# Kernel optimization log

Measured on AMD Instinct MI355X. Metric: run time of the kernel, lower is better.

The kernel has to match this reference:

```python
import jax, jax.numpy as jnp
import numpy as np

WS = 7          # window size
DISP = 3        # WS // 2 cyclic shift displacement
HEADS = 3
HD = 32         # head dim
DIM = 96        # hidden dim (= HEADS*HD)
DS = 4          # patch-merging downscale factor
NWH = 16        # windows per spatial dim after merging (112/7)
SCALE = HD ** -0.5


def _rel_indices(ws):
    idx = np.array([[x, y] for x in range(ws) for y in range(ws)])
    return idx[None, :, :] - idx[:, None, :] + ws - 1  # (ws^2, ws^2, 2)


def _shift_mask(ws, disp, nwh, nww):
    n = ws * ws
    ul = np.zeros((n, n), np.float32)
    ul[-disp * ws:, :-disp * ws] = -np.inf
    ul[:-disp * ws, -disp * ws:] = -np.inf
    lr = np.zeros((ws, ws, ws, ws), np.float32)
    lr[:, -disp:, :, :-disp] = -np.inf
    lr[:, :-disp, :, -disp:] = -np.inf
    lr = lr.reshape(n, n)
    m = np.zeros((nwh * nww, n, n), np.float32)
    m[-nww:] += ul            # last row of windows: upper/lower mask
    m[nww - 1::nww] += lr     # last column of windows: left/right mask
    return m

REL = jnp.asarray(_rel_indices(WS))                       # (49,49,2) int
SHIFT_MASK = jnp.asarray(_shift_mask(WS, DISP, NWH, NWH))  # (256,49,49)


def _layernorm(x, g, b):
    mu = jnp.mean(x, axis=-1, keepdims=True)
    var = jnp.var(x, axis=-1, keepdims=True)
    return (x - mu) * jax.lax.rsqrt(var + 1e-5) * g + b


def _window_attention(y, wqkv, pos_tab, wo, bo, shifted):
    # y: (b, nh, nw, DIM)
    if shifted:
        y = jnp.roll(y, (-DISP, -DISP), axis=(1, 2))
    b, nh, nw, _ = y.shape
    nwh, nww = nh // WS, nw // WS
    qkv = y @ wqkv  # (b, nh, nw, 3*DIM); last dim layout [q|k|v]
    qkv = qkv.reshape(b, nwh, WS, nww, WS, 3, HEADS, HD)
    qkv = qkv.transpose(5, 0, 6, 1, 3, 2, 4, 7).reshape(3, b, HEADS, nwh * nww, WS * WS, HD)
    q, k, v = qkv[0], qkv[1], qkv[2]
    dots = jnp.einsum('bhwid,bhwjd->bhwij', q, k) * SCALE  # (b,h,nwin,49,49)
    dots = dots + pos_tab[REL[..., 0], REL[..., 1]]        # relative pos bias
    if shifted:
        dots = dots + SHIFT_MASK[None, None]
    attn = jax.nn.softmax(dots, axis=-1)
    o = jnp.einsum('bhwij,bhwjd->bhwid', attn, v)
    o = o.reshape(b, HEADS, nwh, nww, WS, WS, HD)
    o = o.transpose(0, 2, 4, 3, 5, 1, 6).reshape(b, nh, nw, HEADS * HD)
    o = o @ wo + bo
    if shifted:
        o = jnp.roll(o, (DISP, DISP), axis=(1, 2))
    return o


def setup_inputs() -> dict:
    key = jax.random.key(0)
    ks = jax.random.split(key, 8)
    B, C, H, W = 16, 3, 448, 448
    s = 0.02
    return {
        'x': jax.random.normal(ks[0], (B, C, H, W), jnp.float32),
        'pm_w': jax.random.normal(ks[1], (C * DS * DS, DIM), jnp.float32) * s,
        'pm_b': jnp.zeros((DIM,), jnp.float32),
        'ln1_g': jnp.ones((2, DIM), jnp.float32),
        'ln1_b': jnp.zeros((2, DIM), jnp.float32),
        'qkv_w': jax.random.normal(ks[2], (2, DIM, 3 * HEADS * HD), jnp.float32) * s,
        'pos': jax.random.normal(ks[3], (2, 2 * WS - 1, 2 * WS - 1), jnp.float32),
        'out_w': jax.random.normal(ks[4], (2, HEADS * HD, DIM), jnp.float32) * s,
        'out_b': jnp.zeros((2, DIM), jnp.float32),
        'ln2_g': jnp.ones((2, DIM), jnp.float32),
        'ln2_b': jnp.zeros((2, DIM), jnp.float32),
        'ff1_w': jax.random.normal(ks[5], (2, DIM, 4 * DIM), jnp.float32) * s,
        'ff1_b': jnp.zeros((2, 4 * DIM), jnp.float32),
        'ff2_w': jax.random.normal(ks[6], (2, 4 * DIM, DIM), jnp.float32) * s,
        'ff2_b': jnp.zeros((2, DIM), jnp.float32),
    }


def reference(x, pm_w, pm_b, ln1_g, ln1_b, qkv_w, pos, out_w, out_b,
              ln2_g, ln2_b, ff1_w, ff1_b, ff2_w, ff2_b):
    b, c, h, w = x.shape
    # PatchMerging: Unfold(k=s=DS) orders channels as (c, kh, kw)
    xp = x.reshape(b, c, h // DS, DS, w // DS, DS)
    xp = xp.transpose(0, 2, 4, 1, 3, 5).reshape(b, h // DS, w // DS, c * DS * DS)
    xp = xp @ pm_w + pm_b  # (b, 112, 112, DIM)
    for i, shifted in enumerate((False, True)):
        y = _layernorm(xp, ln1_g[i], ln1_b[i])
        xp = xp + _window_attention(y, qkv_w[i], pos[i], out_w[i], out_b[i], shifted)
        y = _layernorm(xp, ln2_g[i], ln2_b[i])
        y = jax.nn.gelu(y @ ff1_w[i] + ff1_b[i], approximate=False) @ ff2_w[i] + ff2_b[i]
        xp = xp + y
    return xp.transpose(0, 3, 1, 2)  # (b, DIM, 112, 112)
```

## Files before the change

### kernel.cpp

```cpp
#include <hip/hip_runtime.h>
#include <hip/hip_bf16.h>

#define HW 112
#define NPIX (HW*HW)
#define NTOK_TOTAL (16*NPIX)
#define SCALE_ATTN 0.17677669529663689f

typedef short bf16x8 __attribute__((ext_vector_type(8)));
typedef float f32x4 __attribute__((ext_vector_type(4)));

__device__ __forceinline__ short f2bf(float f) {
    __hip_bfloat16 h = __float2bfloat16(f);
    return *reinterpret_cast<short*>(&h);
}

__device__ __forceinline__ float gelu_tanh(float x) {
    float t  = x * x;
    float m1 = fmaf(0.071354816f, t, 1.5957691f);
    float e  = __expf(x * m1);
    float r  = __builtin_amdgcn_rcpf(e + 1.0f);
    return fmaf(-x, r, x);
}

__global__ __launch_bounds__(256) void patch_merge_kernel(
    const float* __restrict__ x, const float* __restrict__ pm_w,
    const float* __restrict__ pm_b, float* __restrict__ xp)
{
    __shared__ float w_lds[48*96];
    __shared__ float in_lds[16*52];
    __shared__ float b_lds[96];
    const int t = threadIdx.x;
    const int jt = blockIdx.x, i = blockIdx.y, b = blockIdx.z;
    const int j0 = jt * 16;

    for (int e = t; e < 48*96; e += 256) w_lds[e] = pm_w[e];
    if (t < 96) b_lds[t] = pm_b[t];
    for (int e = t; e < 768; e += 256) {
        int r = e >> 6, col = e & 63;
        int c = r >> 2, kh = r & 3;
        float v = x[(((size_t)(b*3 + c))*448 + (4*i + kh))*448 + 4*j0 + col];
        in_lds[(col >> 2)*52 + c*16 + kh*4 + (col & 3)] = v;
    }
    __syncthreads();
    for (int e = t; e < 16*96; e += 256) {
        int pos = e / 96, ch = e % 96;
        float acc = b_lds[ch];
        #pragma unroll
        for (int k = 0; k < 48; ++k)
            acc = fmaf(in_lds[pos*52 + k], w_lds[k*96 + ch], acc);
        xp[((size_t)((b*HW + i)*HW) + j0 + pos)*96 + ch] = acc;
    }
}

__global__ __launch_bounds__(256) void prep_weights_kernel(
    const float* __restrict__ ff1, const float* __restrict__ ff2,
    const float* __restrict__ qkv_w, const float* __restrict__ out_w,
    short* __restrict__ w1T, short* __restrict__ w2T,
    short* __restrict__ qkvT, short* __restrict__ outT)
{
    int i = blockIdx.x * 256 + threadIdx.x;
    if (i < 73728) {
        int l = i / 36864, r = i % 36864, n = r / 96, k = r % 96;
        w1T[i] = f2bf(ff1[(size_t)l*36864 + k*384 + n]);
    } else if (i < 147456) {
        int j = i - 73728;
        int l = j / 36864, r = j % 36864, n = r / 384, k = r % 384;
        w2T[j] = f2bf(ff2[(size_t)l*36864 + k*96 + n]);
    } else if (i < 202752) {
        int j = i - 147456;
        int l = j / 27648, r = j % 27648, n = r / 96, k = r % 96;
        qkvT[j] = f2bf(qkv_w[(size_t)l*27648 + k*288 + n]);
    } else if (i < 221184) {
        int j = i - 202752;
        int l = j / 9216, r = j % 9216, n = r / 96, k = r % 96;
        outT[j] = f2bf(out_w[(size_t)l*9216 + k*96 + n]);
    }
}

template<bool SHIFTED>
__global__ __launch_bounds__(192) void attn_mfma_kernel(
    float* __restrict__ xp,
    const float* __restrict__ ln_g, const float* __restrict__ ln_b,
    const short* __restrict__ qkvT,
    const float* __restrict__ pos_tab,
    const short* __restrict__ outT,
    const float* __restrict__ out_b)
{
    __shared__ short bufA[13824];
    __shared__ short qk_s[13824];
    __shared__ short vT_s[6912];
    __shared__ float pos_l[169];
    __shared__ float ob_s[96];
    __shared__ float lng[96], lnb[96];

    const int t = threadIdx.x;
    const int lane = t & 63;
    const int h = t >> 6;
    const int l15 = lane & 15, lhi = lane >> 4;
    const int wh = blockIdx.x >> 4, ww = blockIdx.x & 15;
    const int b = blockIdx.y;
    const int SH = SHIFTED ? 3 : 0;

    if (t < 169) pos_l[t] = pos_tab[t];
    if (t < 96) { lng[t] = ln_g[t]; lnb[t] = ln_b[t]; ob_s[t] = out_b[t]; }
    __syncthreads();

    {
        const int part = t & 3;
        for (int row = t >> 2; row < 49; row += 48) {
            int ti = (row*37) >> 8, tj = row - ti*7;
            int gi = wh*7 + ti + SH; if (gi >= HW) gi -= HW;
            int gj = ww*7 + tj + SH; if (gj >= HW) gj -= HW;
            const float* src = xp + ((size_t)((b*HW + gi)*HW + gj))*96 + part*24;
            float v[24];
            #pragma unroll
            for (int q4 = 0; q4 < 6; ++q4) {
                float4 vv = *reinterpret_cast<const float4*>(src + q4*4);
                v[q4*4+0]=vv.x; v[q4*4+1]=vv.y; v[q4*4+2]=vv.z; v[q4*4+3]=vv.w;
            }
            float s = 0.f, s2 = 0.f;
            #pragma unroll
            for (int j = 0; j < 24; ++j) { s += v[j]; s2 += v[j]*v[j]; }
            s  += __shfl_xor(s, 1);  s  += __shfl_xor(s, 2);
            s2 += __shfl_xor(s2, 1); s2 += __shfl_xor(s2, 2);
            float mu = s * (1.f/96.f);
            float var = s2 * (1.f/96.f) - mu*mu;
            float rs = rsqrtf(var + 1e-5f);
            unsigned* yw = reinterpret_cast<unsigned*>(bufA) + row*52 + part*12;
            #pragma unroll
            for (int j = 0; j < 12; ++j) {
                int c = part*24 + 2*j;
                float lo = (v[2*j]   - mu)*rs*lng[c]   + lnb[c];
                float hi = (v[2*j+1] - mu)*rs*lng[c+1] + lnb[c+1];
                yw[j] = (unsigned)(unsigned short)f2bf(lo) |
                        ((unsigned)(unsigned short)f2bf(hi) << 16);
            }
        }
        for (int e = t; e < 15*52; e += 192)
            reinterpret_cast<unsigned*>(bufA)[(49 + e/52)*52 + e%52] = 0u;
    }
    __syncthreads();

    {
        f32x4 acc[3][2][4];
        #pragma unroll
        for (int p = 0; p < 3; ++p)
            #pragma unroll
            for (int s = 0; s < 2; ++s)
                #pragma unroll
                for (int m = 0; m < 4; ++m)
                    { acc[p][s][m][0]=0.f; acc[p][s][m][1]=0.f; acc[p][s][m][2]=0.f; acc[p][s][m][3]=0.f; }
        #pragma unroll
        for (int ks = 0; ks < 3; ++ks) {
            bf16x8 a[4];
            #pragma unroll
            for (int m = 0; m < 4; ++m)
                a[m] = *reinterpret_cast<const bf16x8*>(&bufA[(m*16 + l15)*104 + ks*32 + lhi*8]);
            #pragma unroll
            for (int p = 0; p < 3; ++p)
                #pragma unroll
                for (int s = 0; s < 2; ++s) {
                    bf16x8 bf = *reinterpret_cast<const bf16x8*>(
                        qkvT + (p*96 + h*32 + s*16 + l15)*96 + ks*32 + lhi*8);
                    #pragma unroll
                    for (int m = 0; m < 4; ++m)
                        acc[p][s][m] = __builtin_amdgcn_mfma_f32_16x16x32_bf16(
                            a[m], bf, acc[p][s][m], 0, 0, 0);
                }
        }
        #pragma unroll
        for (int p = 0; p < 3; ++p)
            #pragma unroll
            for (int s = 0; s < 2; ++s)
                #pragma unroll
                for (int m = 0; m < 4; ++m)
                    #pragma unroll
                    for (int r = 0; r < 4; ++r) {
                        int tok = m*16 + lhi*4 + r;
                        int c = s*16 + l15;
                        short val = f2bf(acc[p][s][m][r]);
                        if (p == 0)      qk_s[h*4608 + tok*72 + c] = val;
                        else if (p == 1) qk_s[h*4608 + tok*72 + 32 + c] = val;
                        else             vT_s[h*2304 + c*72 + tok] = val;
                    }
    }
    __syncthreads();

    float pv[4][4][4];
    {
        f32x4 sacc[4][4];
        #pragma unroll
        for (int m = 0; m < 4; ++m)
            #pragma unroll
            for (int n = 0; n < 4; ++n)
                { sacc[m][n][0]=0.f; sacc[m][n][1]=0.f; sacc[m][n][2]=0.f; sacc[m][n][3]=0.f; }
        bf16x8 aq[4], bk[4];
        #pragma unroll
        for (int m = 0; m < 4; ++m)
            aq[m] = *reinterpret_cast<const bf16x8*>(&qk_s[h*4608 + (m*16 + l15)*72 + lhi*8]);
        #pragma unroll
        for (int n = 0; n < 4; ++n)
            bk[n] = *reinterpret_cast<const bf16x8*>(&qk_s[h*4608 + (n*16 + l15)*72 + 32 + lhi*8]);
        #pragma unroll
        for (int m = 0; m < 4; ++m)
            #pragma unroll
            for (int n = 0; n < 4; ++n)
                sacc[m][n] = __builtin_amdgcn_mfma_f32_16x16x32_bf16(aq[m], bk[n], sacc[m][n], 0, 0, 0);

        #pragma unroll
        for (int m = 0; m < 4; ++m)
            #pragma unroll
            for (int n = 0; n < 4; ++n)
                #pragma unroll
                for (int r = 0; r < 4; ++r) {
                    int i = m*16 + lhi*4 + r, j = n*16 + l15;
                    float v;
                    if (i >= 49 || j >= 49) v = -1e30f;
                    else {
                        int xi = (i*37) >> 8, yi = i - xi*7;
                        int xj = (j*37) >> 8, yj = j - xj*7;
                        v = sacc[m][n][r]*SCALE_ATTN + pos_l[(xj - xi + 6)*13 + (yj - yi + 6)];
                        if (SHIFTED) {
                            if (wh == 15 && ((xi >= 4) != (xj >= 4))) v = -1e30f;
                            if (ww == 15 && ((yi >= 4) != (yj >= 4))) v = -1e30f;
                        }
                    }
                    pv[m][n][r] = v;
                }
    }
    #pragma unroll
    for (int m = 0; m < 4; ++m)
        #pragma unroll
        for (int r = 0; r < 4; ++r) {
            float mx = fmaxf(fmaxf(pv[m][0][r], pv[m][1][r]), fmaxf(pv[m][2][r], pv[m][3][r]));
            mx = fmaxf(mx, __shfl_xor(mx, 1)); mx = fmaxf(mx, __shfl_xor(mx, 2));
            mx = fmaxf(mx, __shfl_xor(mx, 4)); mx = fmaxf(mx, __shfl_xor(mx, 8));
            float e0 = __expf(pv[m][0][r] - mx), e1 = __expf(pv[m][1][r] - mx);
            float e2 = __expf(pv[m][2][r] - mx), e3 = __expf(pv[m][3][r] - mx);
            float s = e0 + e1 + e2 + e3;
            s += __shfl_xor(s, 1); s += __shfl_xor(s, 2);
            s += __shfl_xor(s, 4); s += __shfl_xor(s, 8);
            float inv = 1.f / s;
            pv[m][0][r] = e0*inv; pv[m][1][r] = e1*inv;
            pv[m][2][r] = e2*inv; pv[m][3][r] = e3*inv;
        }
    #pragma unroll
    for (int m = 0; m < 4; ++m)
        #pragma unroll
        for (int n = 0; n < 4; ++n)
            #pragma unroll
            for (int r = 0; r < 4; ++r)
                bufA[h*4608 + (m*16 + lhi*4 + r)*72 + n*16 + l15] = f2bf(pv[m][n][r]);

    f32x4 oacc[2][4];
    #pragma unroll
    for (int n = 0; n < 2; ++n)
        #pragma unroll
        for (int m = 0; m < 4; ++m)
            { oacc[n][m][0]=0.f; oacc[n][m][1]=0.f; oacc[n][m][2]=0.f; oacc[n][m][3]=0.f; }
    #pragma unroll
    for (int ks = 0; ks < 2; ++ks) {
        bf16x8 ap[4], bv[2];
        #pragma unroll
        for (int m = 0; m < 4; ++m)
            ap[m] = *reinterpret_cast<const bf16x8*>(&bufA[h*4608 + (m*16 + l15)*72 + ks*32 + lhi*8]);
        #pragma unroll
        for (int n = 0; n < 2; ++n)
            bv[n] = *reinterpret_cast<const bf16x8*>(&vT_s[h*2304 + (n*16 + l15)*72 + ks*32 + lhi*8]);
        #pragma unroll
        for (int n = 0; n < 2; ++n)
            #pragma unroll
            for (int m = 0; m < 4; ++m)
                oacc[n][m] = __builtin_amdgcn_mfma_f32_16x16x32_bf16(ap[m], bv[n], oacc[n][m], 0, 0, 0);
    }
    __syncthreads();
    #pragma unroll
    for (int n = 0; n < 2; ++n)
        #pragma unroll
        for (int m = 0; m < 4; ++m)
            #pragma unroll
            for (int r = 0; r < 4; ++r)
                bufA[(m*16 + lhi*4 + r)*104 + h*32 + n*16 + l15] = f2bf(oacc[n][m][r]);
    __syncthreads();

    {
        f32x4 pacc[2][4];
        #pragma unroll
        for (int n = 0; n < 2; ++n)
            #pragma unroll
            for (int m = 0; m < 4; ++m)
                { pacc[n][m][0]=0.f; pacc[n][m][1]=0.f; pacc[n][m][2]=0.f; pacc[n][m][3]=0.f; }
        #pragma unroll
        for (int ks = 0; ks < 3; ++ks) {
            bf16x8 ao[4], bw[2];
            #pragma unroll
            for (int m = 0; m < 4; ++m)
                ao[m] = *reinterpret_cast<const bf16x8*>(&bufA[(m*16 + l15)*104 + ks*32 + lhi*8]);
            #pragma unroll
            for (int n = 0; n < 2; ++n)
                bw[n] = *reinterpret_cast<const bf16x8*>(
                    outT + ((h*2 + n)*16 + l15)*96 + ks*32 + lhi*8);
            #pragma unroll
            for (int n = 0; n < 2; ++n)
                #pragma unroll
                for (int m = 0; m < 4; ++m)
                    pacc[n][m] = __builtin_amdgcn_mfma_f32_16x16x32_bf16(ao[m], bw[n], pacc[n][m], 0, 0, 0);
        }
        #pragma unroll
        for (int m = 0; m < 4; ++m)
            #pragma unroll
            for (int r = 0; r < 4; ++r) {
                int tok = m*16 + lhi*4 + r;
                if (tok < 49) {
                    int ti = (tok*37) >> 8, tj = tok - ti*7;
                    int gi = wh*7 + ti + SH; if (gi >= HW) gi -= HW;
                    int gj = ww*7 + tj + SH; if (gj >= HW) gj -= HW;
                    float* dst = xp + ((size_t)((b*HW + gi)*HW + gj))*96;
                    #pragma unroll
                    for (int n = 0; n < 2; ++n) {
                        int ch = (h*2 + n)*16 + l15;
                        dst[ch] += pacc[n][m][r] + ob_s[ch];
                    }
                }
            }
    }
}

__global__ __launch_bounds__(64) void ff_mfma_kernel(
    float* __restrict__ xp,
    const float* __restrict__ ln_g, const float* __restrict__ ln_b,
    const short* __restrict__ w1T,
    const float* __restrict__ b1,
    const short* __restrict__ w2T,
    const float* __restrict__ b2)
{
    __shared__ short y_s[32*104];
    __shared__ short h_s[32*104];

    const int t = threadIdx.x;
    const int l15 = t & 15, lhi = (t & 63) >> 4;
    const size_t tok0 = (size_t)blockIdx.x * 32;

    {
        const int part = t & 3;
        const int rbase = t >> 2;
        float g[24], bb[24];
        #pragma unroll
        for (int q4 = 0; q4 < 6; ++q4) {
            float4 gv = *reinterpret_cast<const float4*>(ln_g + part*24 + q4*4);
            float4 bv = *reinterpret_cast<const float4*>(ln_b + part*24 + q4*4);
            g[q4*4+0]=gv.x; g[q4*4+1]=gv.y; g[q4*4+2]=gv.z; g[q4*4+3]=gv.w;
            bb[q4*4+0]=bv.x; bb[q4*4+1]=bv.y; bb[q4*4+2]=bv.z; bb[q4*4+3]=bv.w;
        }
        #pragma unroll
        for (int it = 0; it < 2; ++it) {
            int row = it*16 + rbase;
            const float* src = xp + (tok0 + row)*96 + part*24;
            float v[24];
            #pragma unroll
            for (int q4 = 0; q4 < 6; ++q4) {
                float4 vv = *reinterpret_cast<const float4*>(src + q4*4);
                v[q4*4+0]=vv.x; v[q4*4+1]=vv.y; v[q4*4+2]=vv.z; v[q4*4+3]=vv.w;
            }
            float s = 0.f, s2 = 0.f;
            #pragma unroll
            for (int j = 0; j < 24; ++j) { s += v[j]; s2 += v[j]*v[j]; }
            s  += __shfl_xor(s, 1);  s  += __shfl_xor(s, 2);
            s2 += __shfl_xor(s2, 1); s2 += __shfl_xor(s2, 2);
            float mu = s * (1.f/96.f);
            float var = s2 * (1.f/96.f) - mu*mu;
            float rs = rsqrtf(var + 1e-5f);
            unsigned* yw = reinterpret_cast<unsigned*>(y_s) + row*52 + part*12;
            #pragma unroll
            for (int j = 0; j < 12; ++j) {
                float lo = (v[2*j]   - mu)*rs*g[2*j]   + bb[2*j];
                float hi = (v[2*j+1] - mu)*rs*g[2*j+1] + bb[2*j+1];
                yw[j] = (unsigned)(unsigned short)f2bf(lo) |
                        ((unsigned)(unsigned short)f2bf(hi) << 16);
            }
        }
    }
    __syncthreads();

    f32x4 acc2[2][6];
    #pragma unroll
    for (int m = 0; m < 2; ++m)
        #pragma unroll
        for (int n = 0; n < 6; ++n)
            { acc2[m][n][0]=0.f; acc2[m][n][1]=0.f; acc2[m][n][2]=0.f; acc2[m][n][3]=0.f; }

    const int abase = l15*104 + lhi*8;

    #pragma unroll
    for (int c = 0; c < 4; ++c) {
        bf16x8 bw1[3][6];
        #pragma unroll
        for (int ks = 0; ks < 3; ++ks)
            #pragma unroll
            for (int n = 0; n < 6; ++n)
                bw1[ks][n] = *reinterpret_cast<const bf16x8*>(
                    w1T + (c*96 + n*16 + l15)*96 + ks*32 + lhi*8);
        float bias1[6];
        #pragma unroll
        for (int n = 0; n < 6; ++n) bias1[n] = b1[c*96 + n*16 + l15];

        bf16x8 ay[3][2];
        #pragma unroll
        for (int ks = 0; ks < 3; ++ks)
            #pragma unroll
            for (int m = 0; m < 2; ++m)
                ay[ks][m] = *reinterpret_cast<const bf16x8*>(
                    &y_s[abase + m*16*104 + ks*32]);

        f32x4 acc1[2][6];
        #pragma unroll
        for (int m = 0; m < 2; ++m)
            #pragma unroll
            for (int n = 0; n < 6; ++n)
                { acc1[m][n][0]=0.f; acc1[m][n][1]=0.f; acc1[m][n][2]=0.f; acc1[m][n][3]=0.f; }
        #pragma unroll
        for (int ks = 0; ks < 3; ++ks)
            #pragma unroll
            for (int n = 0; n < 6; ++n)
                #pragma unroll
                for (int m = 0; m < 2; ++m)
                    acc1[m][n] = __builtin_amdgcn_mfma_f32_16x16x32_bf16(
                        ay[ks][m], bw1[ks][n], acc1[m][n], 0, 0, 0);

        bf16x8 bw2[3][6];
        #pragma unroll
        for (int ks = 0; ks < 3; ++ks)
            #pragma unroll
            for (int n = 0; n < 6; ++n)
                bw2[ks][n] = *reinterpret_cast<const bf16x8*>(
                    w2T + (n*16 + l15)*384 + c*96 + ks*32 + lhi*8);

        #pragma unroll
        for (int n = 0; n < 6; ++n) {
            #pragma unroll
            for (int m = 0; m < 2; ++m)
                #pragma unroll
                for (int r = 0; r < 4; ++r) {
                    float hv = gelu_tanh(acc1[m][n][r] + bias1[n]);
                    int row = m*16 + lhi*4 + r;
                    h_s[row*104 + n*16 + l15] = f2bf(hv);
                }
        }

        #pragma unroll
        for (int ks = 0; ks < 3; ++ks) {
            bf16x8 ah[2];
            #pragma unroll
            for (int m = 0; m < 2; ++m)
                ah[m] = *reinterpret_cast<const bf16x8*>(
                    &h_s[abase + m*16*104 + ks*32]);
            #pragma unroll
            for (int n = 0; n < 6; ++n)
                #pragma unroll
                for (int m = 0; m < 2; ++m)
                    acc2[m][n] = __builtin_amdgcn_mfma_f32_16x16x32_bf16(
                        ah[m], bw2[ks][n], acc2[m][n], 0, 0, 0);
        }
    }

    float b2v[6];
    #pragma unroll
    for (int n = 0; n < 6; ++n) b2v[n] = b2[n*16 + l15];
    #pragma unroll
    for (int m = 0; m < 2; ++m)
        #pragma unroll
        for (int r = 0; r < 4; ++r) {
            float* dst = xp + (tok0 + m*16 + lhi*4 + r)*96 + l15;
            #pragma unroll
            for (int n = 0; n < 6; ++n)
                dst[n*16] += acc2[m][n][r] + b2v[n];
        }
}

__global__ __launch_bounds__(256) void out_kernel(
    const float* __restrict__ xp, float* __restrict__ out)
{
    __shared__ float tile[64*100];
    const int t = threadIdx.x;
    const int b = blockIdx.y;
    const int p0 = blockIdx.x * 64;
    for (int e = t; e < 64*24; e += 256) {
        int r = e / 24, p = e % 24;
        *reinterpret_cast<float4*>(&tile[r*100 + p*4]) =
            *reinterpret_cast<const float4*>(xp + ((size_t)b*NPIX + p0 + r)*96 + p*4);
    }
    __syncthreads();
    for (int e = t; e < 96*64; e += 256) {
        int ch = e >> 6, p = e & 63;
        out[((size_t)(b*96 + ch))*NPIX + p0 + p] = tile[p*100 + ch];
    }
}

extern "C" void kernel_launch(void* const* d_in, const int* in_sizes, int n_in,
                              void* d_out, int out_size, void* d_ws, size_t ws_size,
                              hipStream_t stream)
{
    (void)in_sizes; (void)n_in; (void)out_size; (void)ws_size;
    const float* x     = (const float*)d_in[0];
    const float* pm_w  = (const float*)d_in[1];
    const float* pm_b  = (const float*)d_in[2];
    const float* ln1_g = (const float*)d_in[3];
    const float* ln1_b = (const float*)d_in[4];
    const float* qkv_w = (const float*)d_in[5];
    const float* pos   = (const float*)d_in[6];
    const float* out_w = (const float*)d_in[7];
    const float* out_b = (const float*)d_in[8];
    const float* ln2_g = (const float*)d_in[9];
    const float* ln2_b = (const float*)d_in[10];
    const float* ff1_w = (const float*)d_in[11];
    const float* ff1_b = (const float*)d_in[12];
    const float* ff2_w = (const float*)d_in[13];
    const float* ff2_b = (const float*)d_in[14];

    float* xp    = (float*)d_ws;
    short* w1T_b = (short*)(xp + (size_t)NTOK_TOTAL * 96);
    short* w2T_b = w1T_b + 2*384*96;
    short* qkvT_b = w2T_b + 2*96*384;
    short* outT_b = qkvT_b + 2*288*96;

    prep_weights_kernel<<<864, 256, 0, stream>>>(ff1_w, ff2_w, qkv_w, out_w,
                                                 w1T_b, w2T_b, qkvT_b, outT_b);
    patch_merge_kernel<<<dim3(7, 112, 16), 256, 0, stream>>>(x, pm_w, pm_b, xp);

    for (int L = 0; L < 2; ++L) {
        if (L == 0)
            attn_mfma_kernel<false><<<dim3(256, 16), 192, 0, stream>>>(
                xp, ln1_g, ln1_b, qkvT_b, pos, outT_b, out_b);
        else
            attn_mfma_kernel<true><<<dim3(256, 16), 192, 0, stream>>>(
                xp, ln1_g + 96, ln1_b + 96, qkvT_b + 27648, pos + 169,
                outT_b + 9216, out_b + 96);
        ff_mfma_kernel<<<6272, 64, 0, stream>>>(
            xp, ln2_g + L*96, ln2_b + L*96,
            w1T_b + (size_t)L*384*96, ff1_b + L*384,
            w2T_b + (size_t)L*96*384, ff2_b + L*96);
    }
    out_kernel<<<dim3(196, 16), 256, 0, stream>>>(xp, (float*)d_out);
}
```

Measured before the change: 596.8 us.

## Stage FF weights in LDS shared by four waves with prefetched fragment layout

```diff
diff --git a/kernel.cpp b/kernel.cpp
--- a/kernel.cpp
+++ b/kernel.cpp
@@ -55,17 +55,27 @@
 __global__ __launch_bounds__(256) void prep_weights_kernel(
     const float* __restrict__ ff1, const float* __restrict__ ff2,
     const float* __restrict__ qkv_w, const float* __restrict__ out_w,
-    short* __restrict__ w1T, short* __restrict__ w2T,
+    short* __restrict__ wF,
     short* __restrict__ qkvT, short* __restrict__ outT)
 {
     int i = blockIdx.x * 256 + threadIdx.x;
-    if (i < 73728) {
-        int l = i / 36864, r = i % 36864, n = r / 96, k = r % 96;
-        w1T[i] = f2bf(ff1[(size_t)l*36864 + k*384 + n]);
-    } else if (i < 147456) {
-        int j = i - 73728;
-        int l = j / 36864, r = j % 36864, n = r / 384, k = r % 384;
-        w2T[j] = f2bf(ff2[(size_t)l*36864 + k*96 + n]);
+    if (i < 147456) {
+        int l = i / 73728, r = i % 73728;
+        int c = r / 18432, r2 = r % 18432;
+        int half = r2 / 9216, r3 = r2 % 9216;
+        int f = r3 / 512, L = (r3 % 512) / 8, j = r3 % 8;
+        int ks = f / 6, n = f % 6;
+        float val;
+        if (half == 0) {
+            int k  = ks*32 + (L >> 4)*8 + j;
+            int ng = c*96 + n*16 + (L & 15);
+            val = ff1[(size_t)l*36864 + (size_t)k*384 + ng];
+        } else {
+            int kg = c*96 + ks*32 + (L >> 4)*8 + j;
+            int ng = n*16 + (L & 15);
+            val = ff2[(size_t)l*36864 + (size_t)kg*96 + ng];
+        }
+        wF[i] = f2bf(val);
     } else if (i < 202752) {
         int j = i - 147456;
         int l = j / 27648, r = j % 27648, n = r / 96, k = r % 96;
@@ -326,61 +336,63 @@
     }
 }
 
-__global__ __launch_bounds__(64) void ff_mfma_kernel(
+__global__ __launch_bounds__(256, 2) void ff_mfma_kernel(
     float* __restrict__ xp,
     const float* __restrict__ ln_g, const float* __restrict__ ln_b,
-    const short* __restrict__ w1T,
+    const short* __restrict__ wF,
     const float* __restrict__ b1,
-    const short* __restrict__ w2T,
     const float* __restrict__ b2)
 {
-    __shared__ short y_s[32*104];
-    __shared__ short h_s[32*104];
+    __shared__ short wbuf[18432];
+    __shared__ short h_s[128*104];
 
     const int t = threadIdx.x;
-    const int l15 = t & 15, lhi = (t & 63) >> 4;
-    const size_t tok0 = (size_t)blockIdx.x * 32;
-
+    const int lane = t & 63;
+    const int wv = t >> 6;
+    const int l15 = lane & 15, lhi = (lane >> 4) & 3;
+    const size_t tok0 = (size_t)blockIdx.x * 128 + wv*32;
+
+    bf16x8 y[2][3];
     {
-        const int part = t & 3;
-        const int rbase = t >> 2;
         float g[24], bb[24];
         #pragma unroll
-        for (int q4 = 0; q4 < 6; ++q4) {
-            float4 gv = *reinterpret_cast<const float4*>(ln_g + part*24 + q4*4);
-            float4 bv = *reinterpret_cast<const float4*>(ln_b + part*24 + q4*4);
-            g[q4*4+0]=gv.x; g[q4*4+1]=gv.y; g[q4*4+2]=gv.z; g[q4*4+3]=gv.w;
-            bb[q4*4+0]=bv.x; bb[q4*4+1]=bv.y; bb[q4*4+2]=bv.z; bb[q4*4+3]=bv.w;
-        }
-        #pragma unroll
-        for (int it = 0; it < 2; ++it) {
-            int row = it*16 + rbase;
-            const float* src = xp + (tok0 + row)*96 + part*24;
+        for (int ks = 0; ks < 3; ++ks)
+            #pragma unroll
+            for (int q = 0; q < 2; ++q) {
+                float4 gv = *reinterpret_cast<const float4*>(ln_g + ks*32 + lhi*8 + q*4);
+                float4 bv = *reinterpret_cast<const float4*>(ln_b + ks*32 + lhi*8 + q*4);
+                g[ks*8+q*4+0]=gv.x; g[ks*8+q*4+1]=gv.y; g[ks*8+q*4+2]=gv.z; g[ks*8+q*4+3]=gv.w;
+                bb[ks*8+q*4+0]=bv.x; bb[ks*8+q*4+1]=bv.y; bb[ks*8+q*4+2]=bv.z; bb[ks*8+q*4+3]=bv.w;
+            }
+        #pragma unroll
+        for (int m = 0; m < 2; ++m) {
+            const float* src = xp + (tok0 + m*16 + l15)*96 + lhi*8;
             float v[24];
             #pragma unroll
-            for (int q4 = 0; q4 < 6; ++q4) {
-                float4 vv = *reinterpret_cast<const float4*>(src + q4*4);
-                v[q4*4+0]=vv.x; v[q4*4+1]=vv.y; v[q4*4+2]=vv.z; v[q4*4+3]=vv.w;
+            for (int ks = 0; ks < 3; ++ks) {
+                float4 a0 = *reinterpret_cast<const float4*>(src + ks*32);
+                float4 a1 = *reinterpret_cast<const float4*>(src + ks*32 + 4);
+                v[ks*8+0]=a0.x; v[ks*8+1]=a0.y; v[ks*8+2]=a0.z; v[ks*8+3]=a0.w;
+                v[ks*8+4]=a1.x; v[ks*8+5]=a1.y; v[ks*8+6]=a1.z; v[ks*8+7]=a1.w;
             }
             float s = 0.f, s2 = 0.f;
             #pragma unroll
             for (int j = 0; j < 24; ++j) { s += v[j]; s2 += v[j]*v[j]; }
-            s  += __shfl_xor(s, 1);  s  += __shfl_xor(s, 2);
-            s2 += __shfl_xor(s2, 1); s2 += __shfl_xor(s2, 2);
+            s  += __shfl_xor(s, 16);  s  += __shfl_xor(s, 32);
+            s2 += __shfl_xor(s2, 16); s2 += __shfl_xor(s2, 32);
             float mu = s * (1.f/96.f);
             float var = s2 * (1.f/96.f) - mu*mu;
             float rs = rsqrtf(var + 1e-5f);
-            unsigned* yw = reinterpret_cast<unsigned*>(y_s) + row*52 + part*12;
-            #pragma unroll
-            for (int j = 0; j < 12; ++j) {
-                float lo = (v[2*j]   - mu)*rs*g[2*j]   + bb[2*j];
-                float hi = (v[2*j+1] - mu)*rs*g[2*j+1] + bb[2*j+1];
-                yw[j] = (unsigned)(unsigned short)f2bf(lo) |
-                        ((unsigned)(unsigned short)f2bf(hi) << 16);
-            }
-        }
-    }
-    __syncthreads();
+            #pragma unroll
+            for (int ks = 0; ks < 3; ++ks) {
+                bf16x8 yy;
+                #pragma unroll
+                for (int j = 0; j < 8; ++j)
+                    yy[j] = f2bf((v[ks*8+j] - mu)*rs*g[ks*8+j] + bb[ks*8+j]);
+                y[m][ks] = yy;
+            }
+        }
+    }
 
     f32x4 acc2[2][6];
     #pragma unroll
@@ -389,28 +401,25 @@
         for (int n = 0; n < 6; ++n)
             { acc2[m][n][0]=0.f; acc2[m][n][1]=0.f; acc2[m][n][2]=0.f; acc2[m][n][3]=0.f; }
 
-    const int abase = l15*104 + lhi*8;
-
-    #pragma unroll
+    uint4 wreg[9];
+    #pragma unroll
+    for (int k = 0; k < 9; ++k)
+        wreg[k] = *reinterpret_cast<const uint4*>(
+            wF + (k*4 + wv)*512 + lane*8);
+
     for (int c = 0; c < 4; ++c) {
-        bf16x8 bw1[3][6];
-        #pragma unroll
-        for (int ks = 0; ks < 3; ++ks)
-            #pragma unroll
-            for (int n = 0; n < 6; ++n)
-                bw1[ks][n] = *reinterpret_cast<const bf16x8*>(
-                    w1T + (c*96 + n*16 + l15)*96 + ks*32 + lhi*8);
-        float bias1[6];
-        #pragma unroll
-        for (int n = 0; n < 6; ++n) bias1[n] = b1[c*96 + n*16 + l15];
-
-        bf16x8 ay[3][2];
-        #pragma unroll
-        for (int ks = 0; ks < 3; ++ks)
-            #pragma unroll
-            for (int m = 0; m < 2; ++m)
-                ay[ks][m] = *reinterpret_cast<const bf16x8*>(
-                    &y_s[abase + m*16*104 + ks*32]);
+        __syncthreads();
+        #pragma unroll
+        for (int k = 0; k < 9; ++k)
+            *reinterpret_cast<uint4*>(&wbuf[(k*4 + wv)*512 + lane*8]) = wreg[k];
+        __syncthreads();
+
+        if (c < 3) {
+            #pragma unroll
+            for (int k = 0; k < 9; ++k)
+                wreg[k] = *reinterpret_cast<const uint4*>(
+                    wF + (c + 1)*18432 + (k*4 + wv)*512 + lane*8);
+        }
 
         f32x4 acc1[2][6];
         #pragma unroll
@@ -421,28 +430,24 @@
         #pragma unroll
         for (int ks = 0; ks < 3; ++ks)
             #pragma unroll
-            for (int n = 0; n < 6; ++n)
+            for (int n = 0; n < 6; ++n) {
+                bf16x8 bw = *reinterpret_cast<const bf16x8*>(
+                    &wbuf[(ks*6 + n)*512 + lane*8]);
                 #pragma unroll
                 for (int m = 0; m < 2; ++m)
                     acc1[m][n] = __builtin_amdgcn_mfma_f32_16x16x32_bf16(
-                        ay[ks][m], bw1[ks][n], acc1[m][n], 0, 0, 0);
-
-        bf16x8 bw2[3][6];
-        #pragma unroll
-        for (int ks = 0; ks < 3; ++ks)
-            #pragma unroll
-            for (int n = 0; n < 6; ++n)
-                bw2[ks][n] = *reinterpret_cast<const bf16x8*>(
-                    w2T + (n*16 + l15)*384 + c*96 + ks*32 + lhi*8);
+                        y[m][ks], bw, acc1[m][n], 0, 0, 0);
+            }
 
         #pragma unroll
         for (int n = 0; n < 6; ++n) {
+            float bias = b1[c*96 + n*16 + l15];
             #pragma unroll
             for (int m = 0; m < 2; ++m)
                 #pragma unroll
                 for (int r = 0; r < 4; ++r) {
-                    float hv = gelu_tanh(acc1[m][n][r] + bias1[n]);
-                    int row = m*16 + lhi*4 + r;
+                    float hv = gelu_tanh(acc1[m][n][r] + bias);
+                    int row = wv*32 + m*16 + lhi*4 + r;
                     h_s[row*104 + n*16 + l15] = f2bf(hv);
                 }
         }
@@ -453,13 +458,16 @@
             #pragma unroll
             for (int m = 0; m < 2; ++m)
                 ah[m] = *reinterpret_cast<const bf16x8*>(
-                    &h_s[abase + m*16*104 + ks*32]);
-            #pragma unroll
-            for (int n = 0; n < 6; ++n)
+                    &h_s[(wv*32 + m*16 + l15)*104 + ks*32 + lhi*8]);
+            #pragma unroll
+            for (int n = 0; n < 6; ++n) {
+                bf16x8 bw = *reinterpret_cast<const bf16x8*>(
+                    &wbuf[9216 + (ks*6 + n)*512 + lane*8]);
                 #pragma unroll
                 for (int m = 0; m < 2; ++m)
                     acc2[m][n] = __builtin_amdgcn_mfma_f32_16x16x32_bf16(
-                        ah[m], bw2[ks][n], acc2[m][n], 0, 0, 0);
+                        ah[m], bw, acc2[m][n], 0, 0, 0);
+            }
         }
     }
 
@@ -518,13 +526,12 @@
     const float* ff2_b = (const float*)d_in[14];
 
     float* xp    = (float*)d_ws;
-    short* w1T_b = (short*)(xp + (size_t)NTOK_TOTAL * 96);
-    short* w2T_b = w1T_b + 2*384*96;
-    short* qkvT_b = w2T_b + 2*96*384;
+    short* wF_b  = (short*)(xp + (size_t)NTOK_TOTAL * 96);
+    short* qkvT_b = wF_b + 147456;
     short* outT_b = qkvT_b + 2*288*96;
 
     prep_weights_kernel<<<864, 256, 0, stream>>>(ff1_w, ff2_w, qkv_w, out_w,
-                                                 w1T_b, w2T_b, qkvT_b, outT_b);
+                                                 wF_b, qkvT_b, outT_b);
     patch_merge_kernel<<<dim3(7, 112, 16), 256, 0, stream>>>(x, pm_w, pm_b, xp);
 
     for (int L = 0; L < 2; ++L) {
@@ -535,10 +542,9 @@
             attn_mfma_kernel<true><<<dim3(256, 16), 192, 0, stream>>>(
                 xp, ln1_g + 96, ln1_b + 96, qkvT_b + 27648, pos + 169,
                 outT_b + 9216, out_b + 96);
-        ff_mfma_kernel<<<6272, 64, 0, stream>>>(
+        ff_mfma_kernel<<<1568, 256, 0, stream>>>(
             xp, ln2_g + L*96, ln2_b + L*96,
-            w1T_b + (size_t)L*384*96, ff1_b + L*384,
-            w2T_b + (size_t)L*96*384, ff2_b + L*96);
+            wF_b + (size_t)L*73728, ff1_b + L*384, ff2_b + L*96);
     }
     out_kernel<<<dim3(196, 16), 256, 0, stream>>>(xp, (float*)d_out);
 }
```

New measurement: 595.6 us. Within noise of the previous version (-0.2%).
